# Kernel tuning notes

Measured on AMD Instinct MI355X. Metric: run time of the kernel, lower is better.

## Reference

```python
import jax, jax.numpy as jnp
import numpy as np
from jax import lax

NEIGHBOR_KERNEL = jnp.array([[1.0, 1.0, 1.0],
                             [1.0, 0.0, 1.0],
                             [1.0, 1.0, 1.0]], dtype=jnp.float32).reshape(1, 1, 3, 3)  # OIHW


def setup_inputs() -> dict:
    key = jax.random.key(0)
    # Binary occupancy grid (cellular automaton state), 4096x4096 fp32
    x = jnp.round(jax.random.uniform(key, (4096, 4096), dtype=jnp.float32))
    return {"x": x, "convs": 32}


def reference(x, convs):
    y = x[None, None, :, :]  # (1,1,H,W) NCHW

    def body(i, y):
        # 3x3 neighbor sum (center excluded), 'same' zero padding
        sums = lax.conv_general_dilated(
            y, NEIGHBOR_KERNEL, window_strides=(1, 1), padding="SAME",
            dimension_numbers=("NCHW", "OIHW", "NCHW"))
        # keep cell only if it has more than 3 live neighbors
        return jnp.where(sums > 3.0, y, jnp.zeros_like(y))

    y = lax.fori_loop(0, convs, body, y)
    return jnp.sum(x) - jnp.sum(y)
```

## Files before the change

### kernel.cpp

```cpp
#include <hip/hip_runtime.h>
#include <cstdint>

#define GRID_N 4096
#define WPR 64
#define NROWS 4096
#define NWORDS (WPR * NROWS)
#define NCELLS (GRID_N * GRID_N)

#define KF 8
#define OUT 16
#define SPAN (OUT + 2 * KF)
#define RPW (SPAN / 8)

#define PACK_BLOCKS 2048

__global__ __launch_bounds__(256) void pack_kernel(const float* __restrict__ x,
                                                   uint64_t* __restrict__ bits,
                                                   unsigned long long* __restrict__ px) {
    int lane = threadIdx.x & 63;
    int wv = threadIdx.x >> 6;
    int gw = blockIdx.x * 4 + wv;
    unsigned long long pc = 0;
    #pragma unroll
    for (int it = 0; it < 8; ++it) {
        int c = gw * 8 + it;
        size_t base = (size_t)c * 256 + lane;
        uint64_t my = 0;
        #pragma unroll
        for (int j = 0; j < 4; ++j) {
            float v = x[base + (size_t)j * 64];
            uint64_t m = __ballot(v > 0.5f);
            if (lane == j) my = m;
        }
        if (lane < 4) {
            bits[(c << 2) + lane] = my;
            pc += (unsigned long long)__popcll(my);
        }
    }
    for (int off = 32; off; off >>= 1) pc += __shfl_down(pc, off, 64);
    __shared__ unsigned long long part[4];
    if (lane == 0) part[wv] = pc;
    __syncthreads();
    if (threadIdx.x == 0)
        px[blockIdx.x] = part[0] + part[1] + part[2] + part[3];
}

__device__ __forceinline__ uint64_t life_row(uint64_t u, uint64_t m, uint64_t d,
                                             int lane) {
    uint64_t t = u ^ m;
    uint64_t s = t ^ d;
    uint64_t c = (u & m) | (d & t);
    uint32_t msgL = (uint32_t)(s >> 63) | (((uint32_t)(c >> 63)) << 1);
    uint32_t msgR = ((uint32_t)s & 1u) | (((uint32_t)c & 1u) << 1);
    uint32_t fromL = __shfl_up(msgL, 1);
    uint32_t fromR = __shfl_down(msgR, 1);
    fromL = (lane == 0) ? 0u : fromL;
    fromR = (lane == 63) ? 0u : fromR;
    uint64_t sL = (s << 1) | (uint64_t)(fromL & 1u);
    uint64_t cL = (c << 1) | (uint64_t)((fromL >> 1) & 1u);
    uint64_t sR = (s >> 1) | ((uint64_t)(fromR & 1u) << 63);
    uint64_t cR = (c >> 1) | ((uint64_t)((fromR >> 1) & 1u) << 63);
    uint64_t t0, t1, u0, u1;
    { uint64_t tt = sL ^ s; t0 = tt ^ sR; t1 = (sL & s) | (sR & tt); }
    { uint64_t tt = cL ^ c; u0 = tt ^ cR; u1 = (cL & c) | (cR & tt); }
    uint64_t p = t1 ^ u0, q = t1 & u0;
    uint64_t pred = (q & u1) | ((q ^ u1) & (p | t0));
    return m & pred;
}

template <bool POP>
__global__ __launch_bounds__(512) void step_kernel(const uint64_t* __restrict__ in,
                                                   uint64_t* __restrict__ out,
                                                   unsigned long long* __restrict__ py) {
    int lane = threadIdx.x & 63;
    int wv = threadIdx.x >> 6;
    int b = blockIdx.x;
    int w4 = wv * RPW;
    int gbase = b * OUT - KF;

    uint64_t r[RPW];
    #pragma unroll
    for (int i = 0; i < RPW; ++i) {
        int gr = gbase + w4 + i;
        r[i] = (gr >= 0 && gr < NROWS) ? in[gr * WPR + lane] : 0ULL;
    }

    __shared__ uint64_t bnd[2][8][2][64];

    #pragma unroll
    for (int g = 1; g <= KF; ++g) {
        int p = g & 1;
        bnd[p][wv][0][lane] = r[0];
        bnd[p][wv][1][lane] = r[RPW - 1];
        __syncthreads();
        uint64_t up   = (wv > 0) ? bnd[p][wv - 1][1][lane] : 0ULL;
        uint64_t down = (wv < 7) ? bnd[p][wv + 1][0][lane] : 0ULL;
        uint64_t prev = up;
        #pragma unroll
        for (int i = 0; i < RPW; ++i) {
            int sr = w4 + i;
            uint64_t nxt = (i < RPW - 1) ? r[i + 1] : down;
            if (sr >= g && sr < SPAN - g) {
                uint64_t nv = life_row(prev, r[i], nxt, lane);
                prev = r[i];
                r[i] = nv;
            } else {
                prev = r[i];
            }
        }
    }

    #pragma unroll
    for (int i = 0; i < RPW; ++i) {
        int sr = w4 + i;
        if (sr >= KF && sr < SPAN - KF)
            out[(b * OUT + sr - KF) * WPR + lane] = r[i];
    }

    if (POP) {
        unsigned long long pc = 0;
        #pragma unroll
        for (int i = 0; i < RPW; ++i) {
            int sr = w4 + i;
            if (sr >= KF && sr < SPAN - KF)
                pc += (unsigned long long)__popcll(r[i]);
        }
        for (int off = 32; off; off >>= 1) pc += __shfl_down(pc, off, 64);
        __shared__ unsigned long long part[8];
        if (lane == 0) part[wv] = pc;
        __syncthreads();
        if (threadIdx.x == 0) {
            unsigned long long s = 0;
            #pragma unroll
            for (int i = 0; i < 8; ++i) s += part[i];
            py[b] = s;
        }
    }
}

__global__ __launch_bounds__(256) void finalize_kernel(const unsigned long long* __restrict__ px,
                                                       const unsigned long long* __restrict__ py,
                                                       float* __restrict__ out) {
    int t = threadIdx.x;
    long long v = 0;
    #pragma unroll
    for (int i = 0; i < PACK_BLOCKS / 256; ++i)
        v += (long long)px[t + i * 256];
    v -= (long long)py[t];
    for (int off = 32; off; off >>= 1) v += __shfl_down(v, off, 64);
    __shared__ long long part[4];
    if ((t & 63) == 0) part[t >> 6] = v;
    __syncthreads();
    if (t == 0) out[0] = (float)(part[0] + part[1] + part[2] + part[3]);
}

extern "C" void kernel_launch(void* const* d_in, const int* in_sizes, int n_in,
                              void* d_out, int out_size, void* d_ws, size_t ws_size,
                              hipStream_t stream) {
    const float* x = (const float*)d_in[0];
    float* out = (float*)d_out;

    uint8_t* ws = (uint8_t*)d_ws;
    uint64_t* buf0 = (uint64_t*)ws;
    uint64_t* buf1 = (uint64_t*)(ws + (size_t)NWORDS * 8);
    unsigned long long* px = (unsigned long long*)(ws + (size_t)2 * NWORDS * 8);
    unsigned long long* py = px + PACK_BLOCKS;

    pack_kernel<<<PACK_BLOCKS, 256, 0, stream>>>(x, buf0, px);

    step_kernel<false><<<NROWS / OUT, 512, 0, stream>>>(buf0, buf1, nullptr);
    step_kernel<false><<<NROWS / OUT, 512, 0, stream>>>(buf1, buf0, nullptr);
    step_kernel<false><<<NROWS / OUT, 512, 0, stream>>>(buf0, buf1, nullptr);
    step_kernel<true ><<<NROWS / OUT, 512, 0, stream>>>(buf1, buf0, py);

    finalize_kernel<<<1, 256, 0, stream>>>(px, py, out);
}
```

Measured before the change: 69.32 us.

## Fuse pack, four step passes and finalize into one cooperative kernel

Replaces six separate kernel launches with a single cooperative kernel that packs the grid, runs four 8-generation rounds separated by grid-wide syncs, and does the final reduction in the last block to finish via an atomic ticket. Middle waves keep their rows in registers across rounds and reload only the halo-affected edge waves from global memory, cutting global reads. This removes launch gaps and inter-kernel drain, at the cost of grid.sync overhead, a memset launch, and packing spread over only 256 blocks, which may lower memory-level parallelism for the 64 MB input read.

Measured after the change: 201.8 us. +191.2%, slower.

```diff
diff --git a/kernel.cpp b/kernel.cpp
--- a/kernel.cpp
+++ b/kernel.cpp
@@ -1,49 +1,20 @@
 #include <hip/hip_runtime.h>
+#include <hip/hip_cooperative_groups.h>
 #include <cstdint>
+
+namespace cg = cooperative_groups;
 
 #define GRID_N 4096
 #define WPR 64
 #define NROWS 4096
 #define NWORDS (WPR * NROWS)
-#define NCELLS (GRID_N * GRID_N)
 
 #define KF 8
 #define OUT 16
 #define SPAN (OUT + 2 * KF)
 #define RPW (SPAN / 8)
-
-#define PACK_BLOCKS 2048
-
-__global__ __launch_bounds__(256) void pack_kernel(const float* __restrict__ x,
-                                                   uint64_t* __restrict__ bits,
-                                                   unsigned long long* __restrict__ px) {
-    int lane = threadIdx.x & 63;
-    int wv = threadIdx.x >> 6;
-    int gw = blockIdx.x * 4 + wv;
-    unsigned long long pc = 0;
-    #pragma unroll
-    for (int it = 0; it < 8; ++it) {
-        int c = gw * 8 + it;
-        size_t base = (size_t)c * 256 + lane;
-        uint64_t my = 0;
-        #pragma unroll
-        for (int j = 0; j < 4; ++j) {
-            float v = x[base + (size_t)j * 64];
-            uint64_t m = __ballot(v > 0.5f);
-            if (lane == j) my = m;
-        }
-        if (lane < 4) {
-            bits[(c << 2) + lane] = my;
-            pc += (unsigned long long)__popcll(my);
-        }
-    }
-    for (int off = 32; off; off >>= 1) pc += __shfl_down(pc, off, 64);
-    __shared__ unsigned long long part[4];
-    if (lane == 0) part[wv] = pc;
-    __syncthreads();
-    if (threadIdx.x == 0)
-        px[blockIdx.x] = part[0] + part[1] + part[2] + part[3];
-}
+#define NBLK (NROWS / OUT)
+#define NTHR 512
 
 __device__ __forceinline__ uint64_t life_row(uint64_t u, uint64_t m, uint64_t d,
                                              int lane) {
@@ -68,90 +39,128 @@
     return m & pred;
 }
 
-template <bool POP>
-__global__ __launch_bounds__(512) void step_kernel(const uint64_t* __restrict__ in,
-                                                   uint64_t* __restrict__ out,
-                                                   unsigned long long* __restrict__ py) {
-    int lane = threadIdx.x & 63;
-    int wv = threadIdx.x >> 6;
-    int b = blockIdx.x;
-    int w4 = wv * RPW;
-    int gbase = b * OUT - KF;
+__global__ __launch_bounds__(NTHR) void mega_kernel(
+        const float* __restrict__ x,
+        uint64_t* __restrict__ buf0, uint64_t* __restrict__ buf1,
+        unsigned long long* __restrict__ px, unsigned long long* __restrict__ py,
+        unsigned int* __restrict__ done, float* __restrict__ out) {
+    cg::grid_group grid = cg::this_grid();
+    const int lane = threadIdx.x & 63;
+    const int wv = threadIdx.x >> 6;
+    const int b = blockIdx.x;
 
-    uint64_t r[RPW];
-    #pragma unroll
-    for (int i = 0; i < RPW; ++i) {
-        int gr = gbase + w4 + i;
-        r[i] = (gr >= 0 && gr < NROWS) ? in[gr * WPR + lane] : 0ULL;
+    __shared__ unsigned long long part[8];
+    __shared__ uint64_t bnd[2][8][2][64];
+    __shared__ unsigned int ticket_s;
+    __shared__ long long fin[4];
+
+    unsigned long long pc = 0;
+    #pragma unroll 4
+    for (int it = 0; it < 32; ++it) {
+        int chunk = b * 256 + wv * 32 + it;
+        size_t base = (size_t)chunk * 256 + lane;
+        uint64_t my = 0;
+        #pragma unroll
+        for (int j = 0; j < 4; ++j) {
+            float v = x[base + (size_t)j * 64];
+            uint64_t mm = __ballot(v > 0.5f);
+            if (lane == j) my = mm;
+        }
+        if (lane < 4) {
+            buf0[(size_t)chunk * 4 + lane] = my;
+            pc += (unsigned long long)__popcll(my);
+        }
+    }
+    for (int off = 32; off; off >>= 1) pc += __shfl_down(pc, off, 64);
+    if (lane == 0) part[wv] = pc;
+    __syncthreads();
+    if (threadIdx.x == 0) {
+        unsigned long long s = 0;
+        #pragma unroll
+        for (int i = 0; i < 8; ++i) s += part[i];
+        px[b] = s;
     }
 
-    __shared__ uint64_t bnd[2][8][2][64];
+    grid.sync();
 
-    #pragma unroll
-    for (int g = 1; g <= KF; ++g) {
-        int p = g & 1;
-        bnd[p][wv][0][lane] = r[0];
-        bnd[p][wv][1][lane] = r[RPW - 1];
-        __syncthreads();
-        uint64_t up   = (wv > 0) ? bnd[p][wv - 1][1][lane] : 0ULL;
-        uint64_t down = (wv < 7) ? bnd[p][wv + 1][0][lane] : 0ULL;
-        uint64_t prev = up;
+    const int w4 = wv * RPW;
+    const int gbase = b * OUT - KF;
+    uint64_t r[RPW];
+
+    for (int round = 0; round < 4; ++round) {
+        const uint64_t* src = (round & 1) ? buf1 : buf0;
+        uint64_t* dst       = (round & 1) ? buf0 : buf1;
+        if (round == 0 || wv < 2 || wv >= 6) {
+            #pragma unroll
+            for (int i = 0; i < RPW; ++i) {
+                int gr = gbase + w4 + i;
+                r[i] = (gr >= 0 && gr < NROWS) ? src[(size_t)gr * WPR + lane]
+                                               : 0ULL;
+            }
+        }
+        #pragma unroll
+        for (int g = 1; g <= KF; ++g) {
+            int p = g & 1;
+            bnd[p][wv][0][lane] = r[0];
+            bnd[p][wv][1][lane] = r[RPW - 1];
+            __syncthreads();
+            uint64_t up   = (wv > 0) ? bnd[p][wv - 1][1][lane] : 0ULL;
+            uint64_t down = (wv < 7) ? bnd[p][wv + 1][0][lane] : 0ULL;
+            uint64_t prev = up;
+            #pragma unroll
+            for (int i = 0; i < RPW; ++i) {
+                int sr = w4 + i;
+                uint64_t nxt = (i < RPW - 1) ? r[i + 1] : down;
+                if (sr >= g && sr < SPAN - g) {
+                    uint64_t nv = life_row(prev, r[i], nxt, lane);
+                    prev = r[i];
+                    r[i] = nv;
+                } else {
+                    prev = r[i];
+                }
+            }
+        }
         #pragma unroll
         for (int i = 0; i < RPW; ++i) {
             int sr = w4 + i;
-            uint64_t nxt = (i < RPW - 1) ? r[i + 1] : down;
-            if (sr >= g && sr < SPAN - g) {
-                uint64_t nv = life_row(prev, r[i], nxt, lane);
-                prev = r[i];
-                r[i] = nv;
-            } else {
-                prev = r[i];
-            }
+            if (sr >= KF && sr < SPAN - KF)
+                dst[(size_t)(b * OUT + sr - KF) * WPR + lane] = r[i];
         }
+        if (round < 3) grid.sync();
     }
 
+    pc = 0;
     #pragma unroll
     for (int i = 0; i < RPW; ++i) {
         int sr = w4 + i;
         if (sr >= KF && sr < SPAN - KF)
-            out[(b * OUT + sr - KF) * WPR + lane] = r[i];
+            pc += (unsigned long long)__popcll(r[i]);
     }
+    for (int off = 32; off; off >>= 1) pc += __shfl_down(pc, off, 64);
+    __syncthreads();
+    if (lane == 0) part[wv] = pc;
+    __syncthreads();
+    if (threadIdx.x == 0) {
+        unsigned long long s = 0;
+        #pragma unroll
+        for (int i = 0; i < 8; ++i) s += part[i];
+        py[b] = s;
+        __threadfence();
+        ticket_s = atomicAdd(done, 1u);
+    }
+    __syncthreads();
 
-    if (POP) {
-        unsigned long long pc = 0;
-        #pragma unroll
-        for (int i = 0; i < RPW; ++i) {
-            int sr = w4 + i;
-            if (sr >= KF && sr < SPAN - KF)
-                pc += (unsigned long long)__popcll(r[i]);
+    if (ticket_s == NBLK - 1) {
+        __threadfence();
+        int t = threadIdx.x;
+        if (t < NBLK) {
+            long long v = (long long)px[t] - (long long)py[t];
+            for (int off = 32; off; off >>= 1) v += __shfl_down(v, off, 64);
+            if ((t & 63) == 0) fin[t >> 6] = v;
         }
-        for (int off = 32; off; off >>= 1) pc += __shfl_down(pc, off, 64);
-        __shared__ unsigned long long part[8];
-        if (lane == 0) part[wv] = pc;
         __syncthreads();
-        if (threadIdx.x == 0) {
-            unsigned long long s = 0;
-            #pragma unroll
-            for (int i = 0; i < 8; ++i) s += part[i];
-            py[b] = s;
-        }
+        if (t == 0) out[0] = (float)(fin[0] + fin[1] + fin[2] + fin[3]);
     }
-}
-
-__global__ __launch_bounds__(256) void finalize_kernel(const unsigned long long* __restrict__ px,
-                                                       const unsigned long long* __restrict__ py,
-                                                       float* __restrict__ out) {
-    int t = threadIdx.x;
-    long long v = 0;
-    #pragma unroll
-    for (int i = 0; i < PACK_BLOCKS / 256; ++i)
-        v += (long long)px[t + i * 256];
-    v -= (long long)py[t];
-    for (int off = 32; off; off >>= 1) v += __shfl_down(v, off, 64);
-    __shared__ long long part[4];
-    if ((t & 63) == 0) part[t >> 6] = v;
-    __syncthreads();
-    if (t == 0) out[0] = (float)(part[0] + part[1] + part[2] + part[3]);
 }
 
 extern "C" void kernel_launch(void* const* d_in, const int* in_sizes, int n_in,
@@ -164,14 +173,13 @@
     uint64_t* buf0 = (uint64_t*)ws;
     uint64_t* buf1 = (uint64_t*)(ws + (size_t)NWORDS * 8);
     unsigned long long* px = (unsigned long long*)(ws + (size_t)2 * NWORDS * 8);
-    unsigned long long* py = px + PACK_BLOCKS;
+    unsigned long long* py = px + NBLK;
+    unsigned int* done = (unsigned int*)(py + NBLK);
 
-    pack_kernel<<<PACK_BLOCKS, 256, 0, stream>>>(x, buf0, px);
+    hipMemsetAsync(done, 0, sizeof(unsigned int), stream);
 
-    step_kernel<false><<<NROWS / OUT, 512, 0, stream>>>(buf0, buf1, nullptr);
-    step_kernel<false><<<NROWS / OUT, 512, 0, stream>>>(buf1, buf0, nullptr);
-    step_kernel<false><<<NROWS / OUT, 512, 0, stream>>>(buf0, buf1, nullptr);
-    step_kernel<true ><<<NROWS / OUT, 512, 0, stream>>>(buf1, buf0, py);
-
-    finalize_kernel<<<1, 256, 0, stream>>>(px, py, out);
+    void* args[] = { (void*)&x, (void*)&buf0, (void*)&buf1,
+                     (void*)&px, (void*)&py, (void*)&done, (void*)&out };
+    hipLaunchCooperativeKernel(reinterpret_cast<void*>(mega_kernel),
+                               dim3(NBLK), dim3(NTHR), args, 0, stream);
 }
```

## Halve rows per block, batch lane shuffles per generation, fuse final reduction

Applied to the files above, without the earlier changes.

The number of output rows per block drops from 16 to 8. This doubles the block count to get more waves per CU, at the cost of more redundant halo-row computation (three rows per wave). Within each generation, the left and right carry bits for all of a wave's rows are packed into one 32-bit message, so each generation needs one shuffle pair instead of one per row. The separate finalize kernel is removed: the last block to finish, found with an atomic ticket counter, does the final reduction. This needs an extra memset launch to reset the counter.

Result: slower. 83.59 us (+20.6%).

```diff
diff --git a/kernel.cpp b/kernel.cpp
--- a/kernel.cpp
+++ b/kernel.cpp
@@ -8,10 +8,10 @@
 #define NCELLS (GRID_N * GRID_N)
 
 #define KF 8
-#define OUT 16
+#define OUT 8
 #define SPAN (OUT + 2 * KF)
 #define RPW (SPAN / 8)
-
+#define NBLK (NROWS / OUT)
 #define PACK_BLOCKS 2048
 
 __global__ __launch_bounds__(256) void pack_kernel(const float* __restrict__ x,
@@ -45,67 +45,75 @@
         px[blockIdx.x] = part[0] + part[1] + part[2] + part[3];
 }
 
-__device__ __forceinline__ uint64_t life_row(uint64_t u, uint64_t m, uint64_t d,
-                                             int lane) {
-    uint64_t t = u ^ m;
-    uint64_t s = t ^ d;
-    uint64_t c = (u & m) | (d & t);
-    uint32_t msgL = (uint32_t)(s >> 63) | (((uint32_t)(c >> 63)) << 1);
-    uint32_t msgR = ((uint32_t)s & 1u) | (((uint32_t)c & 1u) << 1);
-    uint32_t fromL = __shfl_up(msgL, 1);
-    uint32_t fromR = __shfl_down(msgR, 1);
-    fromL = (lane == 0) ? 0u : fromL;
-    fromR = (lane == 63) ? 0u : fromR;
-    uint64_t sL = (s << 1) | (uint64_t)(fromL & 1u);
-    uint64_t cL = (c << 1) | (uint64_t)((fromL >> 1) & 1u);
-    uint64_t sR = (s >> 1) | ((uint64_t)(fromR & 1u) << 63);
-    uint64_t cR = (c >> 1) | ((uint64_t)((fromR >> 1) & 1u) << 63);
-    uint64_t t0, t1, u0, u1;
-    { uint64_t tt = sL ^ s; t0 = tt ^ sR; t1 = (sL & s) | (sR & tt); }
-    { uint64_t tt = cL ^ c; u0 = tt ^ cR; u1 = (cL & c) | (cR & tt); }
-    uint64_t p = t1 ^ u0, q = t1 & u0;
-    uint64_t pred = (q & u1) | ((q ^ u1) & (p | t0));
-    return m & pred;
-}
-
 template <bool POP>
 __global__ __launch_bounds__(512) void step_kernel(const uint64_t* __restrict__ in,
                                                    uint64_t* __restrict__ out,
-                                                   unsigned long long* __restrict__ py) {
-    int lane = threadIdx.x & 63;
-    int wv = threadIdx.x >> 6;
-    int b = blockIdx.x;
-    int w4 = wv * RPW;
-    int gbase = b * OUT - KF;
+                                                   const unsigned long long* __restrict__ px,
+                                                   unsigned long long* __restrict__ py,
+                                                   unsigned int* __restrict__ done,
+                                                   float* __restrict__ res) {
+    const int lane = threadIdx.x & 63;
+    const int wv = threadIdx.x >> 6;
+    const int b = blockIdx.x;
+    const int w4 = wv * RPW;
+    const int gbase = b * OUT - KF;
 
     uint64_t r[RPW];
     #pragma unroll
     for (int i = 0; i < RPW; ++i) {
         int gr = gbase + w4 + i;
-        r[i] = (gr >= 0 && gr < NROWS) ? in[gr * WPR + lane] : 0ULL;
+        r[i] = (gr >= 0 && gr < NROWS) ? in[(size_t)gr * WPR + lane] : 0ULL;
     }
 
     __shared__ uint64_t bnd[2][8][2][64];
 
     #pragma unroll
     for (int g = 1; g <= KF; ++g) {
-        int p = g & 1;
+        const int p = g & 1;
         bnd[p][wv][0][lane] = r[0];
         bnd[p][wv][1][lane] = r[RPW - 1];
         __syncthreads();
-        uint64_t up   = (wv > 0) ? bnd[p][wv - 1][1][lane] : 0ULL;
-        uint64_t down = (wv < 7) ? bnd[p][wv + 1][0][lane] : 0ULL;
-        uint64_t prev = up;
+        uint64_t up = (wv > 0) ? bnd[p][wv - 1][1][lane] : 0ULL;
+        uint64_t dn = (wv < 7) ? bnd[p][wv + 1][0][lane] : 0ULL;
+
+        uint64_t sv[RPW], cv[RPW];
+        #pragma unroll
+        for (int i = 0; i < RPW; ++i) {
+            uint64_t a = (i == 0) ? up : r[i - 1];
+            uint64_t d = (i == RPW - 1) ? dn : r[i + 1];
+            uint64_t m = r[i];
+            uint64_t t = a ^ m;
+            sv[i] = t ^ d;
+            cv[i] = (a & m) | (d & t);
+        }
+
+        uint32_t msgL = 0, msgR = 0;
+        #pragma unroll
+        for (int i = 0; i < RPW; ++i) {
+            msgL |= ((uint32_t)(sv[i] >> 63) & 1u) << (2 * i);
+            msgL |= ((uint32_t)(cv[i] >> 63) & 1u) << (2 * i + 1);
+            msgR |= ((uint32_t)sv[i] & 1u) << (2 * i);
+            msgR |= ((uint32_t)cv[i] & 1u) << (2 * i + 1);
+        }
+        uint32_t fromL = __shfl_up(msgL, 1);
+        uint32_t fromR = __shfl_down(msgR, 1);
+        fromL = (lane == 0) ? 0u : fromL;
+        fromR = (lane == 63) ? 0u : fromR;
+
         #pragma unroll
         for (int i = 0; i < RPW; ++i) {
             int sr = w4 + i;
-            uint64_t nxt = (i < RPW - 1) ? r[i + 1] : down;
             if (sr >= g && sr < SPAN - g) {
-                uint64_t nv = life_row(prev, r[i], nxt, lane);
-                prev = r[i];
-                r[i] = nv;
-            } else {
-                prev = r[i];
+                uint64_t sL = (sv[i] << 1) | (uint64_t)((fromL >> (2 * i)) & 1u);
+                uint64_t cL = (cv[i] << 1) | (uint64_t)((fromL >> (2 * i + 1)) & 1u);
+                uint64_t sR = (sv[i] >> 1) | ((uint64_t)((fromR >> (2 * i)) & 1u) << 63);
+                uint64_t cR = (cv[i] >> 1) | ((uint64_t)((fromR >> (2 * i + 1)) & 1u) << 63);
+                uint64_t t0, t1, u0, u1;
+                { uint64_t tt = sL ^ sv[i]; t0 = tt ^ sR; t1 = (sL & sv[i]) | (sR & tt); }
+                { uint64_t tt = cL ^ cv[i]; u0 = tt ^ cR; u1 = (cL & cv[i]) | (cR & tt); }
+                uint64_t pp = t1 ^ u0, q = t1 & u0;
+                uint64_t pred = (q & u1) | ((q ^ u1) & (pp | t0));
+                r[i] &= pred;
             }
         }
     }
@@ -114,7 +122,7 @@
     for (int i = 0; i < RPW; ++i) {
         int sr = w4 + i;
         if (sr >= KF && sr < SPAN - KF)
-            out[(b * OUT + sr - KF) * WPR + lane] = r[i];
+            out[(size_t)(b * OUT + sr - KF) * WPR + lane] = r[i];
     }
 
     if (POP) {
@@ -127,6 +135,8 @@
         }
         for (int off = 32; off; off >>= 1) pc += __shfl_down(pc, off, 64);
         __shared__ unsigned long long part[8];
+        __shared__ unsigned int ticket_s;
+        __shared__ long long fin[8];
         if (lane == 0) part[wv] = pc;
         __syncthreads();
         if (threadIdx.x == 0) {
@@ -134,24 +144,27 @@
             #pragma unroll
             for (int i = 0; i < 8; ++i) s += part[i];
             py[b] = s;
+            __threadfence();
+            ticket_s = atomicAdd(done, 1u);
+        }
+        __syncthreads();
+        if (ticket_s == NBLK - 1) {
+            __threadfence();
+            int t = threadIdx.x;
+            long long v = (long long)px[t] + (long long)px[t + 512] +
+                          (long long)px[t + 1024] + (long long)px[t + 1536] -
+                          (long long)py[t];
+            for (int off = 32; off; off >>= 1) v += __shfl_down(v, off, 64);
+            if (lane == 0) fin[wv] = v;
+            __syncthreads();
+            if (t == 0) {
+                long long s = 0;
+                #pragma unroll
+                for (int i = 0; i < 8; ++i) s += fin[i];
+                res[0] = (float)s;
+            }
         }
     }
-}
-
-__global__ __launch_bounds__(256) void finalize_kernel(const unsigned long long* __restrict__ px,
-                                                       const unsigned long long* __restrict__ py,
-                                                       float* __restrict__ out) {
-    int t = threadIdx.x;
-    long long v = 0;
-    #pragma unroll
-    for (int i = 0; i < PACK_BLOCKS / 256; ++i)
-        v += (long long)px[t + i * 256];
-    v -= (long long)py[t];
-    for (int off = 32; off; off >>= 1) v += __shfl_down(v, off, 64);
-    __shared__ long long part[4];
-    if ((t & 63) == 0) part[t >> 6] = v;
-    __syncthreads();
-    if (t == 0) out[0] = (float)(part[0] + part[1] + part[2] + part[3]);
 }
 
 extern "C" void kernel_launch(void* const* d_in, const int* in_sizes, int n_in,
@@ -165,13 +178,14 @@
     uint64_t* buf1 = (uint64_t*)(ws + (size_t)NWORDS * 8);
     unsigned long long* px = (unsigned long long*)(ws + (size_t)2 * NWORDS * 8);
     unsigned long long* py = px + PACK_BLOCKS;
+    unsigned int* done = (unsigned int*)(py + NBLK);
+
+    hipMemsetAsync(done, 0, sizeof(unsigned int), stream);
 
     pack_kernel<<<PACK_BLOCKS, 256, 0, stream>>>(x, buf0, px);
 
-    step_kernel<false><<<NROWS / OUT, 512, 0, stream>>>(buf0, buf1, nullptr);
-    step_kernel<false><<<NROWS / OUT, 512, 0, stream>>>(buf1, buf0, nullptr);
-    step_kernel<false><<<NROWS / OUT, 512, 0, stream>>>(buf0, buf1, nullptr);
-    step_kernel<true ><<<NROWS / OUT, 512, 0, stream>>>(buf1, buf0, py);
-
-    finalize_kernel<<<1, 256, 0, stream>>>(px, py, out);
+    step_kernel<false><<<NBLK, 512, 0, stream>>>(buf0, buf1, nullptr, nullptr, nullptr, nullptr);
+    step_kernel<false><<<NBLK, 512, 0, stream>>>(buf1, buf0, nullptr, nullptr, nullptr, nullptr);
+    step_kernel<false><<<NBLK, 512, 0, stream>>>(buf0, buf1, nullptr, nullptr, nullptr, nullptr);
+    step_kernel<true ><<<NBLK, 512, 0, stream>>>(buf1, buf0, px, py, done, out);
 }
```
